# Kernel tuning notes

Measured on AMD Instinct MI355X. Metric: run time of the kernel, lower is better.

## Reference

```python
import jax, jax.numpy as jnp
import numpy as np

F = 128; K = 64; SR_CUT = 10.0
NB = 5; NRI = 3; NRA = 2; NRO = 1
N_ATOMS = 10000; N_PAIRS = 320000


def act(x):
    # shifted softplus: softplus(x) - log(2)
    return jax.nn.softplus(x) - jnp.log(2.0).astype(x.dtype)


def residual(x, W1, b1, W2, b2):
    # PhysNet residual: x + dense2(dense1(act(x))) with activation on dense1
    h = act(act(x) @ W1 + b1)
    return x + h @ W2 + b2


def cutoff_fn(D):
    x = D / SR_CUT
    x3 = x * x * x; x4 = x3 * x; x5 = x4 * x
    return jnp.where(x < 1.0, 1.0 - 6.0 * x5 + 15.0 * x4 - 10.0 * x3, 0.0)


def setup_inputs() -> dict:
    key = jax.random.key(0)
    ks = jax.random.split(key, 24)

    def nrm(k, shape, s=0.05):
        return (jax.random.normal(k, shape) * s).astype(jnp.float32)

    inp = {}
    inp["Z"] = jax.random.randint(ks[0], (N_ATOMS,), 1, 95)
    inp["R"] = (jax.random.normal(ks[1], (N_ATOMS, 3)) * 3.0).astype(jnp.float32)
    inp["idx_i"] = jax.random.randint(ks[2], (N_PAIRS,), 0, N_ATOMS)
    inp["idx_j"] = jax.random.randint(ks[3], (N_PAIRS,), 0, N_ATOMS)
    s3 = float(np.sqrt(3.0))
    inp["embeddings"] = jax.random.uniform(ks[4], (95, F), minval=-s3, maxval=s3).astype(jnp.float32)
    inp["rbf_centers"] = jnp.linspace(1.0, float(np.exp(-SR_CUT)), K).astype(jnp.float32)
    width = (0.5 / ((1.0 - float(np.exp(-SR_CUT))) / K)) ** 2
    inp["rbf_widths"] = jnp.full((K,), width, dtype=jnp.float32)
    inp["k2f_W"] = nrm(ks[5], (NB, K, F))
    inp["Wi"] = nrm(ks[6], (NB, F, F)); inp["bi"] = jnp.zeros((NB, F), jnp.float32)
    inp["Wj"] = nrm(ks[7], (NB, F, F)); inp["bj"] = jnp.zeros((NB, F), jnp.float32)
    inp["ri_W1"] = nrm(ks[8], (NB, NRI, F, F)); inp["ri_b1"] = jnp.zeros((NB, NRI, F), jnp.float32)
    inp["ri_W2"] = nrm(ks[9], (NB, NRI, F, F)); inp["ri_b2"] = jnp.zeros((NB, NRI, F), jnp.float32)
    inp["dW"] = nrm(ks[10], (NB, F, F)); inp["db"] = jnp.zeros((NB, F), jnp.float32)
    inp["u"] = jnp.ones((NB, F), jnp.float32)
    inp["ra_W1"] = nrm(ks[11], (NB, NRA, F, F)); inp["ra_b1"] = jnp.zeros((NB, NRA, F), jnp.float32)
    inp["ra_W2"] = nrm(ks[12], (NB, NRA, F, F)); inp["ra_b2"] = jnp.zeros((NB, NRA, F), jnp.float32)
    inp["ro_W1"] = nrm(ks[13], (NB, NRO, F, F)); inp["ro_b1"] = jnp.zeros((NB, NRO, F), jnp.float32)
    inp["ro_W2"] = nrm(ks[14], (NB, NRO, F, F)); inp["ro_b2"] = jnp.zeros((NB, NRO, F), jnp.float32)
    inp["out_W"] = nrm(ks[15], (NB, F, 2))
    inp["Escale"] = jnp.ones((95,), jnp.float32); inp["Eshift"] = jnp.zeros((95,), jnp.float32)
    inp["Qscale"] = jnp.ones((95,), jnp.float32); inp["Qshift"] = jnp.zeros((95,), jnp.float32)
    return inp


def reference(Z, R, idx_i, idx_j, embeddings, rbf_centers, rbf_widths, k2f_W, Wi, bi, Wj, bj,
              ri_W1, ri_b1, ri_W2, ri_b2, dW, db, u, ra_W1, ra_b1, ra_W2, ra_b2,
              ro_W1, ro_b1, ro_W2, ro_b2, out_W, Escale, Eshift, Qscale, Qshift):
    N = R.shape[0]
    # gather-based interatomic distances: gather -> sub -> sumsq -> relu -> sqrt
    dR = R[idx_i] - R[idx_j]                                   # [P,3]
    Dij = jnp.sqrt(jax.nn.relu(jnp.sum(dR * dR, axis=-1)))     # [P]
    # RBF expansion with smooth cutoff
    rbf = cutoff_fn(Dij)[:, None] * jnp.exp(-rbf_widths * (jnp.exp(-Dij)[:, None] - rbf_centers) ** 2)  # [P,K]
    x = embeddings[Z]                                          # [N,F]
    Ea = jnp.zeros((N,), x.dtype)
    Qa = jnp.zeros((N,), x.dtype)
    nhloss = jnp.zeros((), x.dtype)
    last2 = None
    for b in range(NB):
        # --- interaction layer ---
        g = rbf @ k2f_W[b]                                     # [P,F]
        xa = act(x)
        xi = act(xa @ Wi[b] + bi[b])                           # [N,F]
        xj_feat = act(xa @ Wj[b] + bj[b])                      # [N,F]
        msg = g * xj_feat[idx_j]                               # [P,F] gather + modulate
        m = xi + jax.ops.segment_sum(msg, idx_i, num_segments=N)
        for l in range(NRI):
            m = residual(m, ri_W1[b, l], ri_b1[b, l], ri_W2[b, l], ri_b2[b, l])
        m = act(m)
        x = u[b] * x + m @ dW[b] + db[b]
        for l in range(NRA):
            x = residual(x, ra_W1[b, l], ra_b1[b, l], ra_W2[b, l], ra_b2[b, l])
        # --- output block ---
        o = x
        for l in range(NRO):
            o = residual(o, ro_W1[b, l], ro_b1[b, l], ro_W2[b, l], ro_b2[b, l])
        out = act(o) @ out_W[b]                                # [N,2] -> (Ea, Qa)
        Ea = Ea + out[:, 0]
        Qa = Qa + out[:, 1]
        out2 = out * out
        if b > 0:
            nhloss = nhloss + jnp.mean(out2 / (out2 + last2 + 1e-7))
        last2 = out2
    Ea = Escale[Z] * Ea + Eshift[Z]
    Qa = Qscale[Z] * Qa + Qshift[Z]
    return Ea, Qa, Dij, nhloss
```

## Files before the change

kernel.cpp:

```cpp
#include <hip/hip_runtime.h>

typedef __attribute__((ext_vector_type(8))) short bfrag;
typedef __attribute__((ext_vector_type(4))) float ffrag;

__device__ __forceinline__ unsigned short f2b(float f){
  unsigned int u = __float_as_uint(f);
  return (unsigned short)((u + 0x7FFFu + ((u >> 16) & 1u)) >> 16);
}
__device__ __forceinline__ float actf(float v){
  float e = __builtin_amdgcn_exp2f(-fabsf(v)*1.44269504088896341f);
  return fmaxf(v, 0.f) + __builtin_amdgcn_logf(1.f + e)*0.69314718055994531f - 0.69314718055994531f;
}

__global__ __launch_bounds__(256) void k_zero(float* p, int n){
  int i = blockIdx.x*256 + threadIdx.x;
  if (i < n) p[i] = 0.f;
}

__global__ __launch_bounds__(256) void k_dij_count(
    const float* __restrict__ R, const int* __restrict__ idx_i, const int* __restrict__ idx_j,
    float* __restrict__ DijF, float* __restrict__ Dout, int* __restrict__ counts, int P){
  int p = blockIdx.x*256 + threadIdx.x;
  if (p >= P) return;
  int i = idx_i[p], j = idx_j[p];
  float dx = R[i*3+0] - R[j*3+0];
  float dy = R[i*3+1] - R[j*3+1];
  float dz = R[i*3+2] - R[j*3+2];
  float D = sqrtf(fmaxf(dx*dx + dy*dy + dz*dz, 0.f));
  DijF[p] = D;
  Dout[p] = D;
  atomicAdd(&counts[i], 1);
}

__global__ __launch_bounds__(1024) void k_scan(const int* __restrict__ counts,
    int* __restrict__ cursor, int N){
  __shared__ int wsum[16];
  int tid = threadIdx.x;
  int CH = (N + 1023) >> 10;
  int base = tid * CH;
  int s = 0;
  for (int i = 0; i < CH; ++i){
    int idx = base + i;
    s += (idx < N) ? counts[idx] : 0;
  }
  int lane = tid & 63, w = tid >> 6;
  int v = s;
  #pragma unroll
  for (int off = 1; off < 64; off <<= 1){
    int t = __shfl_up(v, off, 64);
    if (lane >= off) v += t;
  }
  if (lane == 63) wsum[w] = v;
  __syncthreads();
  if (tid < 16){
    int t = wsum[tid];
    int vv = t;
    #pragma unroll
    for (int off = 1; off < 16; off <<= 1){
      int u = __shfl_up(vv, off, 64);
      if (tid >= off) vv += u;
    }
    wsum[tid] = vv - t;
  }
  __syncthreads();
  int run = (v - s) + wsum[w];
  for (int i = 0; i < CH; ++i){
    int idx = base + i;
    if (idx < N){ cursor[idx] = run; run += counts[idx]; }
  }
}

__global__ __launch_bounds__(256) void k_scatter(const int* __restrict__ idx_i,
    const int* __restrict__ idx_j, const float* __restrict__ DijF,
    int* __restrict__ cursor, int* __restrict__ i_s, int* __restrict__ j_s,
    float* __restrict__ D_s, int P){
  int p = blockIdx.x*256 + threadIdx.x;
  if (p >= P) return;
  int i = idx_i[p];
  int pos = atomicAdd(&cursor[i], 1);
  i_s[pos] = i;
  j_s[pos] = idx_j[p];
  D_s[pos] = DijF[p];
}

__global__ __launch_bounds__(256) void k_rbf(
    const float* __restrict__ D_s, const float* __restrict__ cent, const float* __restrict__ wid,
    unsigned short* __restrict__ rbf_s, int P){
  int gid = blockIdx.x*256 + threadIdx.x;
  if (gid >= P*8) return;
  int t = gid >> 3, kg = gid & 7;
  float D = D_s[t];
  float xc = D * 0.1f;
  float cut = 0.f;
  if (xc < 1.f){
    float x3 = xc*xc*xc, x4 = x3*xc, x5 = x4*xc;
    cut = 1.f - 6.f*x5 + 15.f*x4 - 10.f*x3;
  }
  float eD = __builtin_amdgcn_exp2f(-D*1.44269504088896341f);
  bfrag o;
  #pragma unroll
  for (int i = 0; i < 8; ++i){
    int k = kg*8 + i;
    float tt = eD - cent[k];
    float v = cut * __builtin_amdgcn_exp2f(-wid[k]*tt*tt*1.44269504088896341f);
    o[i] = (short)f2b(v);
  }
  *(bfrag*)(rbf_s + (size_t)gid*8) = o;
}

__global__ __launch_bounds__(256) void k_prepAll(
    const float* __restrict__ riW1, const float* __restrict__ riW2,
    const float* __restrict__ dW,   const float* __restrict__ raW1,
    const float* __restrict__ raW2, const float* __restrict__ roW1,
    const float* __restrict__ roW2, const float* __restrict__ Wi,
    const float* __restrict__ Wj,   const float* __restrict__ k2f,
    const float* __restrict__ outW,
    unsigned short* __restrict__ WBall, unsigned short* __restrict__ k2fP,
    unsigned short* __restrict__ outWB){
  int gid = blockIdx.x*256 + threadIdx.x;
  if (gid < 75*2048){
    int i = gid >> 11, r = gid & 2047;
    const float* S;
    int slot;
    if (i < 15)      { S = riW1 + (size_t)i*16384;      slot = (i/3)*15 + 2*(i%3); }
    else if (i < 30) { int j=i-15; S = riW2 + (size_t)j*16384; slot = (j/3)*15 + 2*(j%3) + 1; }
    else if (i < 35) { int j=i-30; S = dW   + (size_t)j*16384; slot = j*15 + 6; }
    else if (i < 45) { int j=i-35; S = raW1 + (size_t)j*16384; slot = (j/2)*15 + 7 + 2*(j%2); }
    else if (i < 55) { int j=i-45; S = raW2 + (size_t)j*16384; slot = (j/2)*15 + 8 + 2*(j%2); }
    else if (i < 60) { int j=i-55; S = roW1 + (size_t)j*16384; slot = j*15 + 11; }
    else if (i < 65) { int j=i-60; S = roW2 + (size_t)j*16384; slot = j*15 + 12; }
    else if (i < 70) { int j=i-65; S = Wi   + (size_t)j*16384; slot = ((j==0)?4:(j-1))*15 + 13; }
    else             { int j=i-70; S = Wj   + (size_t)j*16384; slot = ((j==0)?4:(j-1))*15 + 14; }
    int fr = r >> 6, l = r & 63;
    int T = fr >> 2, k0 = fr & 3;
    int n = T*16 + (l & 15);
    int kbase = k0*32 + (l >> 4)*8;
    unsigned short* D = WBall + ((size_t)slot*2048 + r)*8;
    ushort4 o0, o1;
    o0.x=f2b(S[(kbase+0)*128+n]); o0.y=f2b(S[(kbase+1)*128+n]);
    o0.z=f2b(S[(kbase+2)*128+n]); o0.w=f2b(S[(kbase+3)*128+n]);
    o1.x=f2b(S[(kbase+4)*128+n]); o1.y=f2b(S[(kbase+5)*128+n]);
    o1.z=f2b(S[(kbase+6)*128+n]); o1.w=f2b(S[(kbase+7)*128+n]);
    ((ushort4*)D)[0]=o0; ((ushort4*)D)[1]=o1;
  } else if (gid < 75*2048 + 5120){
    int g = gid - 75*2048;
    int l = g & 63, fr = (g >> 6) & 15, b = g >> 10;
    int tile = fr >> 1, kh = fr & 1;
    const float* src = k2f + (size_t)b*64*128;
    int n = tile*16 + (l & 15);
    int kbase = kh*32 + (l >> 4)*8;
    ushort4 o0, o1;
    o0.x = f2b(src[(kbase+0)*128+n]); o0.y = f2b(src[(kbase+1)*128+n]);
    o0.z = f2b(src[(kbase+2)*128+n]); o0.w = f2b(src[(kbase+3)*128+n]);
    o1.x = f2b(src[(kbase+4)*128+n]); o1.y = f2b(src[(kbase+5)*128+n]);
    o1.z = f2b(src[(kbase+6)*128+n]); o1.w = f2b(src[(kbase+7)*128+n]);
    ushort4* dst = (ushort4*)(k2fP + (size_t)g*8);
    dst[0] = o0; dst[1] = o1;
  } else if (gid < 75*2048 + 5120 + 1280){
    int g = gid - (75*2048 + 5120);
    int b = g >> 8, r = g & 255;
    int l = r & 63;
    int col = l & 15;
    int k0 = r >> 6;
    int kbase = k0*32 + (l >> 4)*8;
    ushort4 o0 = {0,0,0,0}, o1 = {0,0,0,0};
    if (col < 2){
      const float* S = outW + (size_t)b*256;
      o0.x=f2b(S[(kbase+0)*2+col]); o0.y=f2b(S[(kbase+1)*2+col]);
      o0.z=f2b(S[(kbase+2)*2+col]); o0.w=f2b(S[(kbase+3)*2+col]);
      o1.x=f2b(S[(kbase+4)*2+col]); o1.y=f2b(S[(kbase+5)*2+col]);
      o1.z=f2b(S[(kbase+6)*2+col]); o1.w=f2b(S[(kbase+7)*2+col]);
    }
    unsigned short* D = outWB + ((size_t)b*256 + r)*8;
    ((ushort4*)D)[0]=o0; ((ushort4*)D)[1]=o1;
  }
}

__device__ __forceinline__ void mmtile(const unsigned short* tile,
    const unsigned short* __restrict__ WB, int w, int l, ffrag C[4]){
  int m = l & 15, q = l >> 4;
  bfrag A[4];
  #pragma unroll
  for (int k0 = 0; k0 < 4; ++k0)
    A[k0] = *(const bfrag*)(tile + m*136 + k0*32 + q*8);
  #pragma unroll
  for (int tt = 0; tt < 4; ++tt){
    ffrag c = {0.f,0.f,0.f,0.f};
    const bfrag* bp = (const bfrag*)(WB + (((w*4+tt)*4)*64 + l)*8);
    #pragma unroll
    for (int k0 = 0; k0 < 4; ++k0)
      c = __builtin_amdgcn_mfma_f32_16x16x32_bf16(A[k0], bp[k0*64], c, 0, 0, 0);
    C[tt] = c;
  }
}

__global__ __launch_bounds__(128) void k_phase1m(
    const int* __restrict__ Z, const float* __restrict__ emb,
    const unsigned short* __restrict__ WB45,
    const float* __restrict__ bi0, const float* __restrict__ bj0,
    float* __restrict__ x_g, float* __restrict__ m_g, float* __restrict__ xjb_g, int N){
  __shared__ unsigned short tile[16*136];
  int tid = threadIdx.x, w = tid >> 6, l = tid & 63;
  int m = l & 15, q = l >> 4, rbase = blockIdx.x*16;
  #pragma unroll
  for (int r = 0; r < 4; ++r){
    int row = rbase + q*4 + r;
    int z = Z[row];
    #pragma unroll
    for (int tt = 0; tt < 4; ++tt){
      int c = (w*4+tt)*16 + m;
      float v = emb[(size_t)z*128 + c];
      x_g[(size_t)row*128 + c] = v;
      tile[(q*4+r)*136 + c] = f2b(actf(v));
    }
  }
  __syncthreads();
  ffrag C[4];
  mmtile(tile, WB45 + 13*16384, w, l, C);
  #pragma unroll
  for (int tt = 0; tt < 4; ++tt){
    int c = (w*4+tt)*16 + m;
    float bb = bi0[c];
    #pragma unroll
    for (int r = 0; r < 4; ++r)
      m_g[(size_t)(rbase + q*4 + r)*128 + c] = actf(C[tt][r] + bb);
  }
  mmtile(tile, WB45 + 14*16384, w, l, C);
  #pragma unroll
  for (int tt = 0; tt < 4; ++tt){
    int c = (w*4+tt)*16 + m;
    float bb = bj0[c];
    #pragma unroll
    for (int r = 0; r < 4; ++r)
      xjb_g[(size_t)(rbase + q*4 + r)*128 + c] = actf(C[tt][r] + bb);
  }
}

__global__ __launch_bounds__(256) void k_pairmsg2(
    const unsigned short* __restrict__ rbf_s, const unsigned short* __restrict__ k2fP,
    const int* __restrict__ i_s, const int* __restrict__ j_s,
    const float* __restrict__ xj, float* __restrict__ m_g, int P){
  __shared__ float G[4][16*130];
  int tid = threadIdx.x, w = tid >> 6, l = tid & 63;
  float* Gw = &G[w][0];
  bfrag B[16];
  #pragma unroll
  for (int t = 0; t < 8; ++t){
    #pragma unroll
    for (int kh = 0; kh < 2; ++kh)
      B[t*2+kh] = *(const bfrag*)(k2fP + (size_t)((t*2+kh)*64 + l)*8);
  }
  int wstart = (blockIdx.x*4 + w)*128;
  if (wstart >= P) return;
  int row16 = l & 15, quad = l >> 4;
  float a0 = 0.f, a1 = 0.f;
  int iCur = -1;
  bfrag A0 = *(const bfrag*)(rbf_s + (size_t)(wstart + row16)*64 + quad*8);
  bfrag A1 = *(const bfrag*)(rbf_s + (size_t)(wstart + row16)*64 + 32 + quad*8);
  int4 iv[4], jv[4];
  #pragma unroll
  for (int g = 0; g < 4; ++g){
    iv[g] = *(const int4*)(i_s + wstart + g*4);
    jv[g] = *(const int4*)(j_s + wstart + g*4);
  }
  #pragma unroll 1
  for (int bi2 = 0; bi2 < 8; ++bi2){
    int bt = wstart + bi2*16;
    const int* ip = (const int*)iv;
    const int* jp = (const int*)jv;
    float2 xv[16];
    #pragma unroll
    for (int k = 0; k < 16; ++k)
      xv[k] = *(const float2*)(xj + (size_t)jp[k]*128 + 2*l);
    #pragma unroll
    for (int t = 0; t < 8; ++t){
      ffrag C = {0.f,0.f,0.f,0.f};
      C = __builtin_amdgcn_mfma_f32_16x16x32_bf16(A0, B[t*2],   C, 0, 0, 0);
      C = __builtin_amdgcn_mfma_f32_16x16x32_bf16(A1, B[t*2+1], C, 0, 0, 0);
      #pragma unroll
      for (int r = 0; r < 4; ++r)
        Gw[(quad*4+r)*130 + t*16 + row16] = C[r];
    }
    bfrag nA0, nA1;
    int4 niv[4], njv[4];
    if (bi2 < 7){
      int btn = bt + 16;
      nA0 = *(const bfrag*)(rbf_s + (size_t)(btn + row16)*64 + quad*8);
      nA1 = *(const bfrag*)(rbf_s + (size_t)(btn + row16)*64 + 32 + quad*8);
      #pragma unroll
      for (int g = 0; g < 4; ++g){
        niv[g] = *(const int4*)(i_s + btn + g*4);
        njv[g] = *(const int4*)(j_s + btn + g*4);
      }
    }
    #pragma unroll
    for (int k = 0; k < 16; ++k){
      int i = ip[k];
      if (i != iCur){
        if (iCur >= 0){
          unsafeAtomicAdd(&m_g[(size_t)iCur*128 + 2*l],     a0);
          unsafeAtomicAdd(&m_g[(size_t)iCur*128 + 2*l + 1], a1);
        }
        iCur = i; a0 = 0.f; a1 = 0.f;
      }
      float g0 = Gw[k*130 + 2*l], g1 = Gw[k*130 + 2*l + 1];
      a0 = fmaf(g0, xv[k].x, a0);
      a1 = fmaf(g1, xv[k].y, a1);
    }
    if (bi2 < 7){
      A0 = nA0; A1 = nA1;
      #pragma unroll
      for (int g = 0; g < 4; ++g){ iv[g] = niv[g]; jv[g] = njv[g]; }
    }
  }
  if (iCur >= 0){
    unsafeAtomicAdd(&m_g[(size_t)iCur*128 + 2*l],     a0);
    unsafeAtomicAdd(&m_g[(size_t)iCur*128 + 2*l + 1], a1);
  }
}

template<int HASNEXT, int NH>
__global__ __launch_bounds__(512) void k_phase2m(
    float* __restrict__ m_g, float* __restrict__ x_g, float* __restrict__ xjb_g,
    const unsigned short* __restrict__ WBb,
    const float* __restrict__ rib1, const float* __restrict__ rib2,
    const float* __restrict__ db, const float* __restrict__ u,
    const float* __restrict__ rab1, const float* __restrict__ rab2,
    const float* __restrict__ rob1, const float* __restrict__ rob2,
    const float* __restrict__ biN, const float* __restrict__ bjN,
    const unsigned short* __restrict__ outWBb,
    float* __restrict__ Ea, float* __restrict__ Qa,
    float* __restrict__ last2, float* __restrict__ nh, int N){
  __shared__ unsigned short tiles[2][2][16*136];
  __shared__ float biasS[16*128];
  int tid = threadIdx.x, w = tid >> 6, l = tid & 63;
  int m = l & 15, q = l >> 4, rbase = blockIdx.x*32;
  int c = w*16 + m;
  ffrag mC[2], xC[2], C[2];
  float xrow[2][4];
  int cur = 0;
  const int nst = HASNEXT ? 15 : 13;
  const int slotSeq[15] = {0,1,2,3,4,5,6,7,8,9,10,
                           HASNEXT?13:11, HASNEXT?14:12, 11, 12};
  bfrag Bb[2][4];
  #pragma unroll
  for (int k0 = 0; k0 < 4; ++k0)
    Bb[0][k0] = *(const bfrag*)(WBb + (size_t)slotSeq[0]*16384 + (size_t)((w*4+k0)*64 + l)*8);

  if (tid < 128){
    biasS[0*128+tid]  = rib1[tid];
    biasS[1*128+tid]  = rib1[128+tid];
    biasS[2*128+tid]  = rib1[256+tid];
    biasS[3*128+tid]  = rib2[tid];
    biasS[4*128+tid]  = rib2[128+tid];
    biasS[5*128+tid]  = rib2[256+tid];
    biasS[6*128+tid]  = db[tid];
    biasS[7*128+tid]  = u[tid];
    biasS[8*128+tid]  = rab1[tid];
    biasS[9*128+tid]  = rab1[128+tid];
    biasS[10*128+tid] = rab2[tid];
    biasS[11*128+tid] = rab2[128+tid];
    biasS[12*128+tid] = rob1[tid];
    biasS[13*128+tid] = rob2[tid];
    biasS[14*128+tid] = biN[tid];
    biasS[15*128+tid] = bjN[tid];
  }
  #pragma unroll
  for (int h = 0; h < 2; ++h){
    #pragma unroll
    for (int r = 0; r < 4; ++r){
      int row = rbase + h*16 + q*4 + r;
      int rs = row < N ? row : N-1;
      xrow[h][r] = x_g[(size_t)rs*128 + c];
      float v = m_g[(size_t)rs*128 + c];
      mC[h][r] = v;
      tiles[h][0][(q*4+r)*136 + c] = f2b(actf(v));
    }
  }
  #pragma unroll 2
  for (int s = 0; s < nst; ++s){
    __syncthreads();
    if (s+1 < nst){
      #pragma unroll
      for (int k0 = 0; k0 < 4; ++k0)
        Bb[(s+1)&1][k0] = *(const bfrag*)(WBb + (size_t)slotSeq[s+1]*16384 + (size_t)((w*4+k0)*64 + l)*8);
    }
    #pragma unroll
    for (int h = 0; h < 2; ++h){
      const unsigned short* tp = &tiles[h][cur][0];
      ffrag cc = {0.f,0.f,0.f,0.f};
      #pragma unroll
      for (int k0 = 0; k0 < 4; ++k0){
        bfrag A = *(const bfrag*)(tp + m*136 + k0*32 + q*8);
        cc = __builtin_amdgcn_mfma_f32_16x16x32_bf16(A, Bb[s&1][k0], cc, 0, 0, 0);
      }
      C[h] = cc;
    }
    if (HASNEXT && s == 11){
      float bb = biasS[14*128 + c];
      #pragma unroll
      for (int h = 0; h < 2; ++h)
        #pragma unroll
        for (int r = 0; r < 4; ++r){
          int row = rbase + h*16 + q*4 + r;
          if (row < N) m_g[(size_t)row*128 + c] = actf(C[h][r] + bb);
        }
    } else if (HASNEXT && s == 12){
      float bb = biasS[15*128 + c];
      #pragma unroll
      for (int h = 0; h < 2; ++h)
        #pragma unroll
        for (int r = 0; r < 4; ++r){
          int row = rbase + h*16 + q*4 + r;
          if (row < N) xjb_g[(size_t)row*128 + c] = actf(C[h][r] + bb);
        }
    } else if (s == 6){
      float uu = biasS[7*128 + c], bb = biasS[6*128 + c];
      #pragma unroll
      for (int h = 0; h < 2; ++h)
        #pragma unroll
        for (int r = 0; r < 4; ++r){
          float nv = uu*xrow[h][r] + C[h][r] + bb;
          xC[h][r] = nv;
          tiles[h][1-cur][(q*4+r)*136 + c] = f2b(actf(nv));
        }
      cur ^= 1;
    } else if (s == 1 || s == 3 || s == 5){
      float bb = biasS[(3 + (s>>1))*128 + c];
      #pragma unroll
      for (int h = 0; h < 2; ++h)
        #pragma unroll
        for (int r = 0; r < 4; ++r){
          float nv = mC[h][r] + C[h][r] + bb;
          mC[h][r] = nv;
          tiles[h][1-cur][(q*4+r)*136 + c] = f2b(actf(nv));
        }
      cur ^= 1;
    } else if (s == 8 || s == 10){
      float bb = biasS[(10 + ((s-8)>>1))*128 + c];
      #pragma unroll
      for (int h = 0; h < 2; ++h)
        #pragma unroll
        for (int r = 0; r < 4; ++r){
          float nv = xC[h][r] + C[h][r] + bb;
          xC[h][r] = nv;
          tiles[h][1-cur][(q*4+r)*136 + c] = f2b(actf(nv));
          if (HASNEXT && s == 10){
            int row = rbase + h*16 + q*4 + r;
            if (row < N) x_g[(size_t)row*128 + c] = nv;
          }
        }
      cur ^= 1;
    } else if ((HASNEXT && s == 14) || (!HASNEXT && s == 12)){
      float bb = biasS[13*128 + c];
      #pragma unroll
      for (int h = 0; h < 2; ++h)
        #pragma unroll
        for (int r = 0; r < 4; ++r){
          float ov = xC[h][r] + C[h][r] + bb;
          tiles[h][1-cur][(q*4+r)*136 + c] = f2b(actf(ov));
        }
      cur ^= 1;
    } else {
      int bidx = (s==0)?0:(s==2)?1:(s==4)?2:(s==7)?8:(s==9)?9:12;
      float bb = biasS[bidx*128 + c];
      #pragma unroll
      for (int h = 0; h < 2; ++h)
        #pragma unroll
        for (int r = 0; r < 4; ++r)
          tiles[h][1-cur][(q*4+r)*136 + c] = f2b(actf(C[h][r] + bb));
      cur ^= 1;
    }
  }
  __syncthreads();
  if (w < 2){
    const unsigned short* tp = &tiles[w][cur][0];
    bfrag A[4];
    #pragma unroll
    for (int k0 = 0; k0 < 4; ++k0)
      A[k0] = *(const bfrag*)(tp + m*136 + k0*32 + q*8);
    ffrag Ch = {0.f,0.f,0.f,0.f};
    #pragma unroll
    for (int k0 = 0; k0 < 4; ++k0){
      bfrag B = *(const bfrag*)(outWBb + (size_t)(k0*64 + l)*8);
      Ch = __builtin_amdgcn_mfma_f32_16x16x32_bf16(A[k0], B, Ch, 0, 0, 0);
    }
    int col = m;
    if (col < 2){
      float tpa = 0.f;
      #pragma unroll
      for (int r = 0; r < 4; ++r){
        int row = rbase + w*16 + q*4 + r;
        if (row < N){
          float val = Ch[r];
          if (NH){
            if (col == 0) Ea[row] += val; else Qa[row] += val;
          } else {
            if (col == 0) Ea[row]  = val; else Qa[row]  = val;
          }
          float sq = val*val;
          if (NH){
            float lastv = last2[row*2 + col];
            tpa += sq/(sq + lastv + 1e-7f);
          }
          last2[row*2 + col] = sq;
        }
      }
      if (NH) unsafeAtomicAdd(nh, tpa);
    }
  }
}

__global__ __launch_bounds__(256) void k_final(
    const int* __restrict__ Z, const float* __restrict__ Ea, const float* __restrict__ Qa,
    const float* __restrict__ Es, const float* __restrict__ Eh,
    const float* __restrict__ Qs, const float* __restrict__ Qh,
    const float* __restrict__ nh, float* __restrict__ out, int N, int P){
  int n = blockIdx.x*256 + threadIdx.x;
  if (n < N){
    int z = Z[n];
    out[n]   = Es[z]*Ea[n] + Eh[z];
    out[N+n] = Qs[z]*Qa[n] + Qh[z];
  }
  if (blockIdx.x == 0 && threadIdx.x == 0)
    out[(size_t)2*N + P] = nh[0] / (2.f * (float)N);
}

extern "C" void kernel_launch(void* const* d_in, const int* in_sizes, int n_in,
                              void* d_out, int out_size, void* d_ws, size_t ws_size,
                              hipStream_t stream){
  const int N = in_sizes[0];
  const int P = in_sizes[2];
  const int F = 128;

  const int* Z      = (const int*)d_in[0];
  const float* R    = (const float*)d_in[1];
  const int* idx_i  = (const int*)d_in[2];
  const int* idx_j  = (const int*)d_in[3];
  const float* emb  = (const float*)d_in[4];
  const float* cent = (const float*)d_in[5];
  const float* wid  = (const float*)d_in[6];
  const float* k2f  = (const float*)d_in[7];
  const float* Wi   = (const float*)d_in[8];  const float* bi   = (const float*)d_in[9];
  const float* Wj   = (const float*)d_in[10]; const float* bj   = (const float*)d_in[11];
  const float* riW1 = (const float*)d_in[12]; const float* rib1 = (const float*)d_in[13];
  const float* riW2 = (const float*)d_in[14]; const float* rib2 = (const float*)d_in[15];
  const float* dWp  = (const float*)d_in[16]; const float* dbp  = (const float*)d_in[17];
  const float* u    = (const float*)d_in[18];
  const float* raW1 = (const float*)d_in[19]; const float* rab1 = (const float*)d_in[20];
  const float* raW2 = (const float*)d_in[21]; const float* rab2 = (const float*)d_in[22];
  const float* roW1 = (const float*)d_in[23]; const float* rob1 = (const float*)d_in[24];
  const float* roW2 = (const float*)d_in[25]; const float* rob2 = (const float*)d_in[26];
  const float* outW = (const float*)d_in[27];
  const float* Es   = (const float*)d_in[28]; const float* Eh   = (const float*)d_in[29];
  const float* Qs   = (const float*)d_in[30]; const float* Qh   = (const float*)d_in[31];

  char* ws = (char*)d_ws;
  size_t off = 0;
  float* DijF  = (float*)(ws + off); off += (size_t)P*4;
  float* D_s   = (float*)(ws + off); off += (size_t)P*4;
  int*   i_s   = (int*)  (ws + off); off += (size_t)P*4;
  int*   j_s   = (int*)  (ws + off); off += (size_t)P*4;
  unsigned short* rbf_s = (unsigned short*)(ws + off); off += (size_t)P*64*2;
  unsigned short* k2fP  = (unsigned short*)(ws + off); off += (size_t)5*16*64*8*2;
  unsigned short* WBall = (unsigned short*)(ws + off); off += (size_t)75*16384*2;
  unsigned short* outWB = (unsigned short*)(ws + off); off += (size_t)5*2048*2;
  float* x     = (float*)(ws + off); off += (size_t)N*F*4;
  float* xjb   = (float*)(ws + off); off += (size_t)N*F*4;
  float* m     = (float*)(ws + off); off += (size_t)N*F*4;
  float* last2 = (float*)(ws + off); off += (size_t)N*2*4;
  float* Ea    = (float*)(ws + off); off += (size_t)N*4;
  float* Qa    = (float*)(ws + off); off += (size_t)N*4;
  float* nh    = (float*)(ws + off); off += 256;
  int*   counts= (int*)  (ws + off); off += (size_t)N*4;
  int*   cursor= (int*)  (ws + off); off += (size_t)N*4;

  float* outF = (float*)d_out;
  float* Dout = outF + (size_t)2*N;

  const int nzero = N + 64;
  k_zero<<<dim3((nzero+255)/256), dim3(256), 0, stream>>>(nh, nzero);
  k_dij_count<<<dim3((P+255)/256), dim3(256), 0, stream>>>(R, idx_i, idx_j, DijF, Dout, counts, P);
  k_scan<<<dim3(1), dim3(1024), 0, stream>>>(counts, cursor, N);
  k_scatter<<<dim3((P+255)/256), dim3(256), 0, stream>>>(idx_i, idx_j, DijF, cursor, i_s, j_s, D_s, P);
  k_rbf<<<dim3((P*8+255)/256), dim3(256), 0, stream>>>(D_s, cent, wid, rbf_s, P);
  k_prepAll<<<dim3((75*2048 + 5120 + 1280 + 255)/256), dim3(256), 0, stream>>>(
      riW1, riW2, dWp, raW1, raW2, roW1, roW2, Wi, Wj, k2f, outW, WBall, k2fP, outWB);

  const int G16 = (N + 15)/16;
  k_phase1m<<<dim3(G16), dim3(128), 0, stream>>>(Z, emb, WBall + (size_t)4*15*16384,
                                                 bi, bj, x, m, xjb, N);

  const int pmg = (P + 511)/512;
  const int G32 = (N + 31)/32;
  for (int b = 0; b < 5; ++b){
    k_pairmsg2<<<dim3(pmg), dim3(256), 0, stream>>>(rbf_s, k2fP + (size_t)b*16*64*8,
                                                    i_s, j_s, xjb, m, P);
    const unsigned short* WBb = WBall + (size_t)b*15*16384;
    const float* a_rib1 = rib1 + (size_t)b*3*F;
    const float* a_rib2 = rib2 + (size_t)b*3*F;
    const float* a_db   = dbp  + (size_t)b*F;
    const float* a_u    = u    + (size_t)b*F;
    const float* a_rab1 = rab1 + (size_t)b*2*F;
    const float* a_rab2 = rab2 + (size_t)b*2*F;
    const float* a_rob1 = rob1 + (size_t)b*F;
    const float* a_rob2 = rob2 + (size_t)b*F;
    int bn = (b < 4) ? (b+1) : 0;
    const float* a_biN = bi + (size_t)bn*F;
    const float* a_bjN = bj + (size_t)bn*F;
    const unsigned short* oWB = outWB + (size_t)b*2048;
    if (b == 0){
      k_phase2m<1,0><<<dim3(G32), dim3(512), 0, stream>>>(m, x, xjb, WBb,
        a_rib1, a_rib2, a_db, a_u, a_rab1, a_rab2, a_rob1, a_rob2,
        a_biN, a_bjN, oWB, Ea, Qa, last2, nh, N);
    } else if (b < 4){
      k_phase2m<1,1><<<dim3(G32), dim3(512), 0, stream>>>(m, x, xjb, WBb,
        a_rib1, a_rib2, a_db, a_u, a_rab1, a_rab2, a_rob1, a_rob2,
        a_biN, a_bjN, oWB, Ea, Qa, last2, nh, N);
    } else {
      k_phase2m<0,1><<<dim3(G32), dim3(512), 0, stream>>>(m, x, xjb, WBb,
        a_rib1, a_rib2, a_db, a_u, a_rab1, a_rab2, a_rob1, a_rob2,
        a_biN, a_bjN, oWB, Ea, Qa, last2, nh, N);
    }
  }
  k_final<<<dim3((N+255)/256), dim3(256), 0, stream>>>(Z, Ea, Qa, Es, Eh, Qs, Qh, nh, outF, N, P);
}
```

Before: 509.2 us.

## Store gathered xj features as bf16 and prefetch next gather a batch ahead

The per-atom xj feature buffer written by the phase kernels is now stored as bf16 instead of fp32, which halves the bytes gathered per pair in the message kernel. The pair-message kernel also software-pipelines the gather: it loads the next batch's indices first, then issues the next batch's xj gathers before consuming the current one, so gather latency overlaps with MFMA and accumulation work. This costs extra registers and adds bf16 rounding to the gathered features.

```diff
diff --git a/kernel.cpp b/kernel.cpp
--- a/kernel.cpp
+++ b/kernel.cpp
@@ -6,6 +6,12 @@
 __device__ __forceinline__ unsigned short f2b(float f){
   unsigned int u = __float_as_uint(f);
   return (unsigned short)((u + 0x7FFFu + ((u >> 16) & 1u)) >> 16);
+}
+__device__ __forceinline__ float b2f_lo(unsigned int v){
+  return __uint_as_float(v << 16);
+}
+__device__ __forceinline__ float b2f_hi(unsigned int v){
+  return __uint_as_float(v & 0xFFFF0000u);
 }
 __device__ __forceinline__ float actf(float v){
   float e = __builtin_amdgcn_exp2f(-fabsf(v)*1.44269504088896341f);
@@ -198,7 +204,7 @@
     const int* __restrict__ Z, const float* __restrict__ emb,
     const unsigned short* __restrict__ WB45,
     const float* __restrict__ bi0, const float* __restrict__ bj0,
-    float* __restrict__ x_g, float* __restrict__ m_g, float* __restrict__ xjb_g, int N){
+    float* __restrict__ x_g, float* __restrict__ m_g, unsigned short* __restrict__ xjb_g, int N){
   __shared__ unsigned short tile[16*136];
   int tid = threadIdx.x, w = tid >> 6, l = tid & 63;
   int m = l & 15, q = l >> 4, rbase = blockIdx.x*16;
@@ -232,14 +238,14 @@
     float bb = bj0[c];
     #pragma unroll
     for (int r = 0; r < 4; ++r)
-      xjb_g[(size_t)(rbase + q*4 + r)*128 + c] = actf(C[tt][r] + bb);
+      xjb_g[(size_t)(rbase + q*4 + r)*128 + c] = f2b(actf(C[tt][r] + bb));
   }
 }
 
 __global__ __launch_bounds__(256) void k_pairmsg2(
     const unsigned short* __restrict__ rbf_s, const unsigned short* __restrict__ k2fP,
     const int* __restrict__ i_s, const int* __restrict__ j_s,
-    const float* __restrict__ xj, float* __restrict__ m_g, int P){
+    const unsigned short* __restrict__ xj, float* __restrict__ m_g, int P){
   __shared__ float G[4][16*130];
   int tid = threadIdx.x, w = tid >> 6, l = tid & 63;
   float* Gw = &G[w][0];
@@ -263,15 +269,26 @@
     iv[g] = *(const int4*)(i_s + wstart + g*4);
     jv[g] = *(const int4*)(j_s + wstart + g*4);
   }
+  unsigned int xv[16];
+  {
+    const int* jp = (const int*)jv;
+    #pragma unroll
+    for (int k = 0; k < 16; ++k)
+      xv[k] = *(const unsigned int*)(xj + (size_t)jp[k]*128 + 2*l);
+  }
   #pragma unroll 1
   for (int bi2 = 0; bi2 < 8; ++bi2){
     int bt = wstart + bi2*16;
     const int* ip = (const int*)iv;
-    const int* jp = (const int*)jv;
-    float2 xv[16];
-    #pragma unroll
-    for (int k = 0; k < 16; ++k)
-      xv[k] = *(const float2*)(xj + (size_t)jp[k]*128 + 2*l);
+    int4 niv[4], njv[4];
+    if (bi2 < 7){
+      int btn = bt + 16;
+      #pragma unroll
+      for (int g = 0; g < 4; ++g){
+        niv[g] = *(const int4*)(i_s + btn + g*4);
+        njv[g] = *(const int4*)(j_s + btn + g*4);
+      }
+    }
     #pragma unroll
     for (int t = 0; t < 8; ++t){
       ffrag C = {0.f,0.f,0.f,0.f};
@@ -282,16 +299,15 @@
         Gw[(quad*4+r)*130 + t*16 + row16] = C[r];
     }
     bfrag nA0, nA1;
-    int4 niv[4], njv[4];
+    unsigned int nxv[16];
     if (bi2 < 7){
       int btn = bt + 16;
       nA0 = *(const bfrag*)(rbf_s + (size_t)(btn + row16)*64 + quad*8);
       nA1 = *(const bfrag*)(rbf_s + (size_t)(btn + row16)*64 + 32 + quad*8);
-      #pragma unroll
-      for (int g = 0; g < 4; ++g){
-        niv[g] = *(const int4*)(i_s + btn + g*4);
-        njv[g] = *(const int4*)(j_s + btn + g*4);
-      }
+      const int* njp = (const int*)njv;
+      #pragma unroll
+      for (int k = 0; k < 16; ++k)
+        nxv[k] = *(const unsigned int*)(xj + (size_t)njp[k]*128 + 2*l);
     }
     #pragma unroll
     for (int k = 0; k < 16; ++k){
@@ -304,13 +320,15 @@
         iCur = i; a0 = 0.f; a1 = 0.f;
       }
       float g0 = Gw[k*130 + 2*l], g1 = Gw[k*130 + 2*l + 1];
-      a0 = fmaf(g0, xv[k].x, a0);
-      a1 = fmaf(g1, xv[k].y, a1);
+      a0 = fmaf(g0, b2f_lo(xv[k]), a0);
+      a1 = fmaf(g1, b2f_hi(xv[k]), a1);
     }
     if (bi2 < 7){
       A0 = nA0; A1 = nA1;
       #pragma unroll
       for (int g = 0; g < 4; ++g){ iv[g] = niv[g]; jv[g] = njv[g]; }
+      #pragma unroll
+      for (int k = 0; k < 16; ++k) xv[k] = nxv[k];
     }
   }
   if (iCur >= 0){
@@ -321,7 +339,7 @@
 
 template<int HASNEXT, int NH>
 __global__ __launch_bounds__(512) void k_phase2m(
-    float* __restrict__ m_g, float* __restrict__ x_g, float* __restrict__ xjb_g,
+    float* __restrict__ m_g, float* __restrict__ x_g, unsigned short* __restrict__ xjb_g,
     const unsigned short* __restrict__ WBb,
     const float* __restrict__ rib1, const float* __restrict__ rib2,
     const float* __restrict__ db, const float* __restrict__ u,
@@ -412,7 +430,7 @@
         #pragma unroll
         for (int r = 0; r < 4; ++r){
           int row = rbase + h*16 + q*4 + r;
-          if (row < N) xjb_g[(size_t)row*128 + c] = actf(C[h][r] + bb);
+          if (row < N) xjb_g[(size_t)row*128 + c] = f2b(actf(C[h][r] + bb));
         }
     } else if (s == 6){
       float uu = biasS[7*128 + c], bb = biasS[6*128 + c];
@@ -566,7 +584,7 @@
   unsigned short* WBall = (unsigned short*)(ws + off); off += (size_t)75*16384*2;
   unsigned short* outWB = (unsigned short*)(ws + off); off += (size_t)5*2048*2;
   float* x     = (float*)(ws + off); off += (size_t)N*F*4;
-  float* xjb   = (float*)(ws + off); off += (size_t)N*F*4;
+  unsigned short* xjb = (unsigned short*)(ws + off); off += (size_t)N*F*2;
   float* m     = (float*)(ws + off); off += (size_t)N*F*4;
   float* last2 = (float*)(ws + off); off += (size_t)N*2*4;
   float* Ea    = (float*)(ws + off); off += (size_t)N*4;
```

New measurement: 493.1 us. -3.2%, faster.
